# Optimization experiments

Hardware: AMD Instinct MI355X
Metric: run time of the kernel (lower is better)

Reference implementation:

```python
import jax, jax.numpy as jnp
import numpy as np

B, S, HID, HEADS = 8, 1024, 1024, 16
DK = HID // HEADS


def setup_inputs() -> dict:
    key = jax.random.key(0)
    ks = jax.random.split(key, 6)
    scale = 1.0 / np.sqrt(HID)
    return {
        "q": jax.random.normal(ks[0], (B, S, HID), jnp.float32),
        "k": jax.random.normal(ks[1], (B, S, HID), jnp.float32),
        "v": jax.random.normal(ks[2], (B, S, HID), jnp.float32),
        "Wq": jax.random.normal(ks[3], (HID, HID), jnp.float32) * scale,
        "Wk": jax.random.normal(ks[4], (HID, HID), jnp.float32) * scale,
        "Wv": jax.random.normal(ks[5], (HID, HID), jnp.float32) * scale,
        "mask": 1,
    }


def _split_heads(x):
    # [B, S, HID] -> [B, HEADS, S, DK]
    b, s, _ = x.shape
    return x.reshape(b, s, HEADS, DK).transpose(0, 2, 1, 3)


def reference(q, k, v, Wq, Wk, Wv, mask):
    # torch nn.Linear: y = x @ W.T (no bias)
    qh = _split_heads(q @ Wq.T)
    kh = _split_heads(k @ Wk.T)
    vh = _split_heads(v @ Wv.T)

    scores = jnp.einsum("bhqd,bhkd->bhqk", qh, kh) / jnp.sqrt(jnp.asarray(DK, qh.dtype))
    scores = jax.nn.softmax(scores, axis=-1)
    if mask:
        # original zeroes entries where row > col AFTER softmax (keeps upper triangle)
        tri = jnp.triu(jnp.ones((S, S), scores.dtype))
        scores = scores * tri
        # original then transposes the (masked) score matrix before applying to V
        scores = scores.transpose(0, 1, 3, 2)
    out = jnp.einsum("bhqk,bhkd->bhqd", scores, vh)
    # [B, HEADS, S, DK] -> [B, S, HID]
    return out.transpose(0, 2, 1, 3).reshape(q.shape[0], -1, HID)
```

## Files before the change

kernel.cpp:

```cpp
#include <hip/hip_runtime.h>
#include <math.h>

#define B 8
#define S 1024
#define HID 1024
#define HEADS 16
#define DK 64

typedef unsigned short u16;
typedef unsigned int u32;
typedef _Float16 f16;
typedef __attribute__((ext_vector_type(8))) _Float16 half8;
typedef __attribute__((ext_vector_type(4))) _Float16 half4;
typedef __attribute__((ext_vector_type(2))) _Float16 half2;
typedef __attribute__((ext_vector_type(2))) __fp16 fp16x2;
typedef __attribute__((ext_vector_type(4))) float f32x4;

#define GLL16(G, L)                                                         \
    __builtin_amdgcn_global_load_lds(                                       \
        (const __attribute__((address_space(1))) u32*)(G),                  \
        (__attribute__((address_space(3))) u32*)(L), 16, 0, 0)

__device__ __forceinline__ float exp_s(float c) {
#if __has_builtin(__builtin_amdgcn_exp2f)
    return __builtin_amdgcn_exp2f(c * 0.18033688f);
#else
    return __expf(c * 0.125f);
#endif
}

__global__ __launch_bounds__(256) void cast_all(
    const float* __restrict__ q, const float* __restrict__ k,
    const float* __restrict__ v, const float* __restrict__ Wq,
    const float* __restrict__ Wk, const float* __restrict__ Wv,
    f16* __restrict__ oq, f16* __restrict__ ok, f16* __restrict__ ov,
    f16* __restrict__ owq, f16* __restrict__ owk, f16* __restrict__ owv) {
    const size_t SZ = (size_t)B * S * HID;
    const size_t WZ = (size_t)HID * HID;
    size_t e = ((size_t)blockIdx.x * 256 + threadIdx.x) * 8;
    const float* src;
    f16* dst;
    if (e < SZ)               { src = q + e;               dst = oq + e; }
    else if (e < 2 * SZ)      { src = k + (e - SZ);        dst = ok + (e - SZ); }
    else if (e < 3 * SZ)      { src = v + (e - 2 * SZ);    dst = ov + (e - 2 * SZ); }
    else if (e < 3 * SZ + WZ) { src = Wq + (e - 3 * SZ);   dst = owq + (e - 3 * SZ); }
    else if (e < 3 * SZ + 2 * WZ) { src = Wk + (e - 3 * SZ - WZ); dst = owk + (e - 3 * SZ - WZ); }
    else                      { src = Wv + (e - 3 * SZ - 2 * WZ); dst = owv + (e - 3 * SZ - 2 * WZ); }
    f32x4 a = *(const f32x4*)src;
    f32x4 b = *(const f32x4*)(src + 4);
    half8 h;
    h[0] = (f16)a[0]; h[1] = (f16)a[1]; h[2] = (f16)a[2]; h[3] = (f16)a[3];
    h[4] = (f16)b[0]; h[5] = (f16)b[1]; h[6] = (f16)b[2]; h[7] = (f16)b[3];
    *(half8*)dst = h;
}

__global__ __launch_bounds__(256) void proj_mfma_b(
    const f16* __restrict__ Xq, const f16* __restrict__ Xk,
    const f16* __restrict__ Xv, const f16* __restrict__ Wq,
    const f16* __restrict__ Wk, const f16* __restrict__ Wv,
    f16* __restrict__ Qb, f16* __restrict__ Kb, f16* __restrict__ Vt) {
    const int z = blockIdx.x % 3;
    const int cx = blockIdx.x / 3;
    const f16* __restrict__ X = (z == 0) ? Xq : (z == 1) ? Xk : Xv;
    const f16* __restrict__ W = (z == 0) ? Wq : (z == 1) ? Wk : Wv;

    __shared__ u16 As[128 * 32];
    __shared__ u16 Bs[128 * 32];
    const int tid = threadIdx.x;
    const int wv = tid >> 6, ln = tid & 63;
    const int lr = ln & 15, quad = ln >> 4;
    const int wm = wv >> 1, wn = wv & 1;
    const int row0 = blockIdx.y * 128, col0 = cx * 128;

    const int srow = tid >> 2;
    const int sch = tid & 3;

    f32x4 acc[4][4];
    #pragma unroll
    for (int i = 0; i < 4; ++i)
        #pragma unroll
        for (int j = 0; j < 4; ++j) acc[i][j] = (f32x4){0.f, 0.f, 0.f, 0.f};

    for (int k0 = 0; k0 < HID; k0 += 32) {
        #pragma unroll
        for (int p = 0; p < 2; ++p) {
            int r = p * 64 + srow;
            int csw = sch ^ ((r >> 1) & 3);
            GLL16(X + (size_t)(row0 + r) * HID + k0 + csw * 8, As + p * 2048 + tid * 8);
            GLL16(W + (size_t)(col0 + r) * HID + k0 + csw * 8, Bs + p * 2048 + tid * 8);
        }
        __syncthreads();
        half8 a[4], b[4];
        #pragma unroll
        for (int mi = 0; mi < 4; ++mi) {
            int r = wm * 64 + mi * 16 + lr;
            a[mi] = *(const half8*)(As + r * 32 + ((quad ^ ((r >> 1) & 3)) * 8));
        }
        #pragma unroll
        for (int ni = 0; ni < 4; ++ni) {
            int r = wn * 64 + ni * 16 + lr;
            b[ni] = *(const half8*)(Bs + r * 32 + ((quad ^ ((r >> 1) & 3)) * 8));
        }
        #pragma unroll
        for (int mi = 0; mi < 4; ++mi)
            #pragma unroll
            for (int ni = 0; ni < 4; ++ni)
                acc[mi][ni] = __builtin_amdgcn_mfma_f32_16x16x32_f16(
                    a[mi], b[ni], acc[mi][ni], 0, 0, 0);
        __syncthreads();
    }

    if (z < 2) {
        f16* __restrict__ Y = (z == 0) ? Qb : Kb;
        #pragma unroll
        for (int mi = 0; mi < 4; ++mi) {
            int m = row0 + wm * 64 + mi * 16 + quad * 4;
            #pragma unroll
            for (int ni = 0; ni < 4; ++ni) {
                int n = col0 + wn * 64 + ni * 16 + lr;
                #pragma unroll
                for (int r = 0; r < 4; ++r)
                    Y[(size_t)(m + r) * HID + n] = (f16)acc[mi][ni][r];
            }
        }
    } else {
        #pragma unroll
        for (int mi = 0; mi < 4; ++mi) {
            int m = row0 + wm * 64 + mi * 16 + quad * 4;
            int bb = m >> 10, s = m & 1023;
            #pragma unroll
            for (int ni = 0; ni < 4; ++ni) {
                int n = col0 + wn * 64 + ni * 16 + lr;
                half4 h4;
                #pragma unroll
                for (int r = 0; r < 4; ++r) h4[r] = (f16)acc[mi][ni][r];
                *(half4*)(Vt + ((size_t)(bb * 16 + (n >> 6)) * 64 + (n & 63)) * S + s) = h4;
            }
        }
    }
}

__global__ __launch_bounds__(256) void stats_mfma(const f16* __restrict__ Q,
                                                  const f16* __restrict__ K,
                                                  f16* __restrict__ Vt) {
    const int bh = blockIdx.x, jt = blockIdx.y;
    const int b = bh >> 4, h = bh & 15;
    const int tid = threadIdx.x;
    const int wv = tid >> 6, ln = tid & 63;
    const int lr = ln & 15, quad = ln >> 4;
    __shared__ u16 Ks[64 * 64];
    __shared__ float rlL[64];

    const int j = jt * 64 + wv * 16 + lr;
    const f16* qrow = Q + (size_t)(b * S + j) * HID + h * 64;
    half8 aq0 = *(const half8*)(qrow + quad * 8);
    half8 aq1 = *(const half8*)(qrow + 32 + quad * 8);

    float sl[4] = {0.f, 0.f, 0.f, 0.f};

    for (int i0 = 0; i0 < S; i0 += 64) {
        __syncthreads();
        #pragma unroll
        for (int p = 0; p < 2; ++p) {
            int r = p * 32 + (tid >> 3);
            int csw = (tid & 7) ^ (r & 7);
            GLL16(K + (size_t)(b * S + i0 + r) * HID + h * 64 + csw * 8,
                  Ks + p * 2048 + tid * 8);
        }
        __syncthreads();
        #pragma unroll
        for (int isub = 0; isub < 4; ++isub) {
            int il = isub * 16 + lr;
            half8 bk0 = *(const half8*)(Ks + il * 64 + (((0 + quad) ^ (il & 7)) * 8));
            half8 bk1 = *(const half8*)(Ks + il * 64 + (((4 + quad) ^ (il & 7)) * 8));
            f32x4 c = {0.f, 0.f, 0.f, 0.f};
            c = __builtin_amdgcn_mfma_f32_16x16x32_f16(aq0, bk0, c, 0, 0, 0);
            c = __builtin_amdgcn_mfma_f32_16x16x32_f16(aq1, bk1, c, 0, 0, 0);
            #pragma unroll
            for (int r = 0; r < 4; ++r) sl[r] += exp_s(c[r]);
        }
    }

    #pragma unroll
    for (int r = 0; r < 4; ++r) {
        float v = sl[r];
        v += __shfl_xor(v, 1, 64);
        v += __shfl_xor(v, 2, 64);
        v += __shfl_xor(v, 4, 64);
        v += __shfl_xor(v, 8, 64);
        if (lr == 0) rlL[wv * 16 + quad * 4 + r] = 1.0f / v;
    }
    __syncthreads();

    {
        const int d = tid >> 2, cg = (tid & 3) * 16;
        f16* vrow = Vt + (size_t)(bh * 64 + d) * S + jt * 64 + cg;
        #pragma unroll
        for (int c8 = 0; c8 < 2; ++c8) {
            half8 hv = *(half8*)(vrow + c8 * 8);
            #pragma unroll
            for (int e = 0; e < 8; ++e)
                hv[e] = (f16)((float)hv[e] * rlL[cg + c8 * 8 + e]);
            *(half8*)(vrow + c8 * 8) = hv;
        }
    }
}

__global__ __launch_bounds__(256) void apply_mfma(const f16* __restrict__ Q,
                                                  const f16* __restrict__ K,
                                                  const f16* __restrict__ Vt,
                                                  float* __restrict__ out) {
    const int bh = blockIdx.x;
    const int it2 = (gridDim.y - 1) - blockIdx.y;
    const int b = bh >> 4, h = bh & 15;
    const int tid = threadIdx.x;
    const int wv = tid >> 6, ln = tid & 63;
    const int lr = ln & 15, quad = ln >> 4;
    const int i0b = it2 * 128;
    const int i0w = i0b + wv * 32;

    __shared__ u16 Qs[64 * 64];
    __shared__ u16 Vts[64 * 64];

    half8 bk[2][2];
    #pragma unroll
    for (int isub = 0; isub < 2; ++isub) {
        int i = i0w + isub * 16 + lr;
        #pragma unroll
        for (int kf = 0; kf < 2; ++kf)
            bk[isub][kf] = *(const half8*)(K + (size_t)(b * S + i) * HID + h * 64 +
                                           kf * 32 + quad * 8);
    }

    f32x4 acc[4][2];
    #pragma unroll
    for (int nt = 0; nt < 4; ++nt)
        #pragma unroll
        for (int isub = 0; isub < 2; ++isub) acc[nt][isub] = (f32x4){0.f, 0.f, 0.f, 0.f};

    const int nch = 2 * it2 + 2;
    for (int jc = 0; jc < nch; ++jc) {
        const int j0 = jc * 64;
        __syncthreads();
        #pragma unroll
        for (int p = 0; p < 2; ++p) {
            int r = p * 32 + (tid >> 3);
            int csw = (tid & 7) ^ (r & 7);
            GLL16(Q + (size_t)(b * S + j0 + r) * HID + h * 64 + csw * 8,
                  Qs + p * 2048 + tid * 8);
        }
        #pragma unroll
        for (int p = 0; p < 2; ++p) {
            int d = p * 32 + (tid >> 3);
            int csw = (tid & 7) ^ (d & 7);
            GLL16(Vt + (size_t)(bh * 64 + d) * S + j0 + csw * 8,
                  Vts + p * 2048 + tid * 8);
        }
        __syncthreads();

        #pragma unroll
        for (int jsub = 0; jsub < 4; ++jsub) {
            const int jbase = j0 + jsub * 16;
            if (jbase > i0w + 31) break;

            const int jl = jsub * 16 + lr;
            half8 aq0 = *(const half8*)(Qs + jl * 64 + (((0 + quad) ^ (jl & 7)) * 8));
            half8 aq1 = *(const half8*)(Qs + jl * 64 + (((4 + quad) ^ (jl & 7)) * 8));
            half4 av[4];
            #pragma unroll
            for (int nt = 0; nt < 4; ++nt) {
                int d = nt * 16 + lr;
                int ch = (jsub * 2 + (quad >> 1)) ^ (d & 7);
                av[nt] = *(const half4*)(Vts + d * 64 + ch * 8 + (quad & 1) * 4);
            }

            #pragma unroll
            for (int isub = 0; isub < 2; ++isub) {
                const int ib = i0w + isub * 16;
                if (jbase > ib + 15) continue;
                f32x4 c = {0.f, 0.f, 0.f, 0.f};
                c = __builtin_amdgcn_mfma_f32_16x16x32_f16(aq0, bk[isub][0], c, 0, 0, 0);
                c = __builtin_amdgcn_mfma_f32_16x16x32_f16(aq1, bk[isub][1], c, 0, 0, 0);
                float w0 = exp_s(c[0]), w1 = exp_s(c[1]);
                float w2 = exp_s(c[2]), w3 = exp_s(c[3]);
                if (jbase + 15 > ib) {
                    const int i_col = ib + lr;
                    const int jq = jbase + quad * 4;
                    if (jq + 0 > i_col) w0 = 0.f;
                    if (jq + 1 > i_col) w1 = 0.f;
                    if (jq + 2 > i_col) w2 = 0.f;
                    if (jq + 3 > i_col) w3 = 0.f;
                }
                fp16x2 q0 = __builtin_amdgcn_cvt_pkrtz(w0, w1);
                fp16x2 q1 = __builtin_amdgcn_cvt_pkrtz(w2, w3);
                half2 p0 = __builtin_bit_cast(half2, q0);
                half2 p1 = __builtin_bit_cast(half2, q1);
                half4 bw;
                bw[0] = p0[0]; bw[1] = p0[1]; bw[2] = p1[0]; bw[3] = p1[1];
                #pragma unroll
                for (int nt = 0; nt < 4; ++nt)
                    acc[nt][isub] = __builtin_amdgcn_mfma_f32_16x16x16f16(
                        av[nt], bw, acc[nt][isub], 0, 0, 0);
            }
        }
    }

    #pragma unroll
    for (int isub = 0; isub < 2; ++isub) {
        int i = i0w + isub * 16 + lr;
        #pragma unroll
        for (int nt = 0; nt < 4; ++nt)
            *(f32x4*)(out + (size_t)(b * S + i) * HID + h * 64 + nt * 16 + quad * 4) =
                acc[nt][isub];
    }
}

extern "C" void kernel_launch(void* const* d_in, const int* in_sizes, int n_in,
                              void* d_out, int out_size, void* d_ws, size_t ws_size,
                              hipStream_t stream) {
    const float* q  = (const float*)d_in[0];
    const float* k  = (const float*)d_in[1];
    const float* v  = (const float*)d_in[2];
    const float* Wq = (const float*)d_in[3];
    const float* Wk = (const float*)d_in[4];
    const float* Wv = (const float*)d_in[5];

    const size_t SZ = (size_t)B * S * HID;
    const size_t WZ = (size_t)HID * HID;

    f16* xq = (f16*)d_out;
    f16* xk = xq + SZ;

    char* p = (char*)d_ws;
    f16* xv = (f16*)p;      p += SZ * 2;
    f16* wq = (f16*)p;      p += WZ * 2;
    f16* wk = (f16*)p;      p += WZ * 2;
    f16* wv_ = (f16*)p;     p += WZ * 2;
    f16* Qb = (f16*)p;      p += SZ * 2;
    f16* Kb = (f16*)p;      p += SZ * 2;
    f16* Vt = (f16*)p;      p += SZ * 2;

    float* out = (float*)d_out;

    const int ncast = (int)((3 * SZ + 3 * WZ) / 8 / 256);
    cast_all<<<ncast, 256, 0, stream>>>(q, k, v, Wq, Wk, Wv,
                                        xq, xk, xv, wq, wk, wv_);

    proj_mfma_b<<<dim3(3 * HID / 128, (B * S) / 128), 256, 0, stream>>>(
        xq, xk, xv, wq, wk, wv_, Qb, Kb, Vt);

    stats_mfma<<<dim3(B * HEADS, S / 64), 256, 0, stream>>>(Qb, Kb, Vt);
    apply_mfma<<<dim3(B * HEADS, S / 128), 256, 0, stream>>>(Qb, Kb, Vt, out);
}
```

Measured before the change: 298.3 us.

## Remap projection blocks for XCD locality and double stats tile per block

The projection launch becomes a 1D grid whose block index is remapped so that blocks landing on the same XCD (assuming round-robin dispatch across 8 XCDs) share X row tiles and W column tiles, aiming to improve L2 reuse. The stats kernel now handles 128 query rows per block instead of 64, so each K tile loaded into LDS is reused by two MFMA row groups, halving K traffic and the block count. The cost is more registers per thread and fewer blocks in the stats kernel.

```diff
diff --git a/kernel.cpp b/kernel.cpp
--- a/kernel.cpp
+++ b/kernel.cpp
@@ -59,8 +59,14 @@
     const f16* __restrict__ Xv, const f16* __restrict__ Wq,
     const f16* __restrict__ Wk, const f16* __restrict__ Wv,
     f16* __restrict__ Qb, f16* __restrict__ Kb, f16* __restrict__ Vt) {
-    const int z = blockIdx.x % 3;
-    const int cx = blockIdx.x / 3;
+    const int L = blockIdx.x;
+    const int xcd = L & 7;
+    const int w8 = L >> 3;
+    const int cx = w8 & 7;
+    const int g = xcd * 24 + (w8 >> 3);
+    const int z = g % 3;
+    const int ytile = g / 3;
+
     const f16* __restrict__ X = (z == 0) ? Xq : (z == 1) ? Xk : Xv;
     const f16* __restrict__ W = (z == 0) ? Wq : (z == 1) ? Wk : Wv;
 
@@ -70,7 +76,7 @@
     const int wv = tid >> 6, ln = tid & 63;
     const int lr = ln & 15, quad = ln >> 4;
     const int wm = wv >> 1, wn = wv & 1;
-    const int row0 = blockIdx.y * 128, col0 = cx * 128;
+    const int row0 = ytile * 128, col0 = cx * 128;
 
     const int srow = tid >> 2;
     const int sch = tid & 3;
@@ -149,14 +155,18 @@
     const int wv = tid >> 6, ln = tid & 63;
     const int lr = ln & 15, quad = ln >> 4;
     __shared__ u16 Ks[64 * 64];
-    __shared__ float rlL[64];
-
-    const int j = jt * 64 + wv * 16 + lr;
-    const f16* qrow = Q + (size_t)(b * S + j) * HID + h * 64;
-    half8 aq0 = *(const half8*)(qrow + quad * 8);
-    half8 aq1 = *(const half8*)(qrow + 32 + quad * 8);
-
-    float sl[4] = {0.f, 0.f, 0.f, 0.f};
+    __shared__ float rlL[128];
+
+    half8 aq[2][2];
+    #pragma unroll
+    for (int jsub = 0; jsub < 2; ++jsub) {
+        const int j = jt * 128 + wv * 32 + jsub * 16 + lr;
+        const f16* qrow = Q + (size_t)(b * S + j) * HID + h * 64;
+        aq[jsub][0] = *(const half8*)(qrow + quad * 8);
+        aq[jsub][1] = *(const half8*)(qrow + 32 + quad * 8);
+    }
+
+    float sl[2][4] = {};
 
     for (int i0 = 0; i0 < S; i0 += 64) {
         __syncthreads();
@@ -173,30 +183,35 @@
             int il = isub * 16 + lr;
             half8 bk0 = *(const half8*)(Ks + il * 64 + (((0 + quad) ^ (il & 7)) * 8));
             half8 bk1 = *(const half8*)(Ks + il * 64 + (((4 + quad) ^ (il & 7)) * 8));
-            f32x4 c = {0.f, 0.f, 0.f, 0.f};
-            c = __builtin_amdgcn_mfma_f32_16x16x32_f16(aq0, bk0, c, 0, 0, 0);
-            c = __builtin_amdgcn_mfma_f32_16x16x32_f16(aq1, bk1, c, 0, 0, 0);
-            #pragma unroll
-            for (int r = 0; r < 4; ++r) sl[r] += exp_s(c[r]);
-        }
-    }
-
-    #pragma unroll
-    for (int r = 0; r < 4; ++r) {
-        float v = sl[r];
-        v += __shfl_xor(v, 1, 64);
-        v += __shfl_xor(v, 2, 64);
-        v += __shfl_xor(v, 4, 64);
-        v += __shfl_xor(v, 8, 64);
-        if (lr == 0) rlL[wv * 16 + quad * 4 + r] = 1.0f / v;
-    }
+            #pragma unroll
+            for (int jsub = 0; jsub < 2; ++jsub) {
+                f32x4 c = {0.f, 0.f, 0.f, 0.f};
+                c = __builtin_amdgcn_mfma_f32_16x16x32_f16(aq[jsub][0], bk0, c, 0, 0, 0);
+                c = __builtin_amdgcn_mfma_f32_16x16x32_f16(aq[jsub][1], bk1, c, 0, 0, 0);
+                #pragma unroll
+                for (int r = 0; r < 4; ++r) sl[jsub][r] += exp_s(c[r]);
+            }
+        }
+    }
+
+    #pragma unroll
+    for (int jsub = 0; jsub < 2; ++jsub)
+        #pragma unroll
+        for (int r = 0; r < 4; ++r) {
+            float v = sl[jsub][r];
+            v += __shfl_xor(v, 1, 64);
+            v += __shfl_xor(v, 2, 64);
+            v += __shfl_xor(v, 4, 64);
+            v += __shfl_xor(v, 8, 64);
+            if (lr == 0) rlL[wv * 32 + jsub * 16 + quad * 4 + r] = 1.0f / v;
+        }
     __syncthreads();
 
     {
-        const int d = tid >> 2, cg = (tid & 3) * 16;
-        f16* vrow = Vt + (size_t)(bh * 64 + d) * S + jt * 64 + cg;
-        #pragma unroll
-        for (int c8 = 0; c8 < 2; ++c8) {
+        const int d = tid >> 2, cg = (tid & 3) * 32;
+        f16* vrow = Vt + (size_t)(bh * 64 + d) * S + jt * 128 + cg;
+        #pragma unroll
+        for (int c8 = 0; c8 < 4; ++c8) {
             half8 hv = *(half8*)(vrow + c8 * 8);
             #pragma unroll
             for (int e = 0; e < 8; ++e)
@@ -346,9 +361,8 @@
     cast_all<<<ncast, 256, 0, stream>>>(q, k, v, Wq, Wk, Wv,
                                         xq, xk, xv, wq, wk, wv_);
 
-    proj_mfma_b<<<dim3(3 * HID / 128, (B * S) / 128), 256, 0, stream>>>(
-        xq, xk, xv, wq, wk, wv_, Qb, Kb, Vt);
-
-    stats_mfma<<<dim3(B * HEADS, S / 64), 256, 0, stream>>>(Qb, Kb, Vt);
+    proj_mfma_b<<<1536, 256, 0, stream>>>(xq, xk, xv, wq, wk, wv_, Qb, Kb, Vt);
+
+    stats_mfma<<<dim3(B * HEADS, S / 128), 256, 0, stream>>>(Qb, Kb, Vt);
     apply_mfma<<<dim3(B * HEADS, S / 128), 256, 0, stream>>>(Qb, Kb, Vt, out);
 }
```

New measurement: 290.1 us. 2.8% less time.
